# Kernel optimization log

Measured on AMD Instinct MI355X. Metric: run time of the kernel, lower is better.

## Reference

```python
import jax, jax.numpy as jnp
import numpy as np

S_, H_, W_ = 7, 56, 56   # input_resolution
WS = 7                   # window_size
SHIFT = 3                # shift_size
GT = 1                   # gt_num (global tokens per window)
HEADS = 12
EPS = 1e-5


def _rel_pos_index(w):
    # replicates the torch buffer construction (incl. its 3*w-1 / 2*w-1 multipliers)
    coords = np.stack(np.meshgrid(np.arange(w), np.arange(w), np.arange(w), indexing='ij'))
    cf = coords.reshape(3, -1)
    rc = (cf[:, :, None] - cf[:, None, :]).transpose(1, 2, 0).astype(np.int64)
    rc += w - 1
    rc[..., 0] *= 3 * w - 1
    rc[..., 1] *= 2 * w - 1
    return rc.sum(-1)  # (w^3, w^3)


def _attn_mask(S, H, W, w, sh):
    # standard 3D shifted-window mask, built once from static shapes
    img = np.zeros((S, H, W))
    cnt = 0
    sls = (slice(0, -w), slice(-w, -sh), slice(-sh, None))
    for a in sls:
        for b in sls:
            for c in sls:
                img[a, b, c] = cnt
                cnt += 1
    m = img.reshape(S // w, w, H // w, w, W // w, w).transpose(0, 2, 4, 1, 3, 5).reshape(-1, w ** 3)
    d = m[:, None, :] - m[:, :, None]
    return np.where(d != 0, -100.0, 0.0).astype(np.float32)  # (nW, w^3, w^3)


def _ln(x, g, b):
    mu = jnp.mean(x, -1, keepdims=True)
    var = jnp.mean((x - mu) ** 2, -1, keepdims=True)
    return (x - mu) * jax.lax.rsqrt(var + EPS) * g + b


def setup_inputs() -> dict:
    key = jax.random.key(0)
    ks = jax.random.split(key, 7)
    C = 384
    hid = 4 * C
    L = S_ * H_ * W_
    nW = (S_ // WS) * (H_ // WS) * (W_ // WS)
    p = lambda k, shape: jax.random.normal(k, shape, jnp.float32) * 0.02
    return dict(
        x=jax.random.normal(ks[0], (1, L, C), jnp.float32),
        gt=jax.random.normal(ks[1], (nW, GT, C), jnp.float32),
        norm1_g=jnp.ones((C,), jnp.float32), norm1_b=jnp.zeros((C,), jnp.float32),
        qkv_w=p(ks[2], (C, 3 * C)), qkv_b=jnp.zeros((3 * C,), jnp.float32),
        bias_table=p(ks[3], ((2 * WS - 1) ** 3, HEADS)),
        proj_w=p(ks[4], (C, C)), proj_b=jnp.zeros((C,), jnp.float32),
        norm2_g=jnp.ones((C,), jnp.float32), norm2_b=jnp.zeros((C,), jnp.float32),
        fc1_w=p(ks[5], (C, hid)), fc1_b=jnp.zeros((hid,), jnp.float32),
        fc2_w=p(ks[6], (hid, C)), fc2_b=jnp.zeros((C,), jnp.float32),
    )


def _forward(x, gt, norm1_g, norm1_b, qkv_w, qkv_b, bias_table, proj_w, proj_b,
             norm2_g, norm2_b, fc1_w, fc1_b, fc2_w, fc2_b):
    B, L, C = x.shape
    h = HEADS
    d = C // h
    scale = d ** -0.5
    N_ = WS ** 3
    N = N_ + GT
    rpi = _rel_pos_index(WS)
    mask = jnp.asarray(_attn_mask(S_, H_, W_, WS, SHIFT))
    nW = mask.shape[0]

    shortcut = x
    xs = _ln(x, norm1_g, norm1_b).reshape(B, S_, H_, W_, C)
    xs = jnp.roll(xs, (-SHIFT, -SHIFT, -SHIFT), axis=(1, 2, 3))  # cyclic shift
    # window partition -> (B*nW, N_, C)
    xw = xs.reshape(B, S_ // WS, WS, H_ // WS, WS, W_ // WS, WS, C)
    xw = xw.transpose(0, 1, 3, 5, 2, 4, 6, 7).reshape(-1, N_, C)

    # --- WindowAttention with global tokens ---
    xc = jnp.concatenate([gt, xw], axis=1)  # (B*nW, N, C)
    qkv = (xc @ qkv_w + qkv_b).reshape(-1, N, 3, h, d).transpose(2, 0, 3, 1, 4)
    q, k, v = qkv[0] * scale, qkv[1], qkv[2]  # (B*nW, h, N, d)
    attn = jnp.einsum('bhnd,bhmd->bhnm', q, k)
    bias = bias_table[rpi.reshape(-1)].reshape(N_, N_, h).transpose(2, 0, 1)  # (h, N_, N_)
    bias = jnp.pad(bias, ((0, 0), (GT, 0), (GT, 0)))      # zeros on gt rows/cols == original submatrix add
    mpad = jnp.pad(mask, ((0, 0), (GT, 0), (GT, 0)))
    attn = attn + bias[None]
    attn = attn.reshape(B, nW, h, N, N) + mpad[None, :, None]
    attn = jax.nn.softmax(attn.reshape(-1, h, N, N), axis=-1)
    out = jnp.einsum('bhnm,bhmd->bhnd', attn, v).transpose(0, 2, 1, 3).reshape(-1, N, C)
    out = out @ proj_w + proj_b
    gt_out = out[:, :GT]
    xw = out[:, GT:]

    # window reverse + reverse shift
    xs = xw.reshape(B, S_ // WS, H_ // WS, W_ // WS, WS, WS, WS, C)
    xs = xs.transpose(0, 1, 4, 2, 5, 3, 6, 7).reshape(B, S_, H_, W_, C)
    xs = jnp.roll(xs, (SHIFT, SHIFT, SHIFT), axis=(1, 2, 3)).reshape(B, L, C)

    x = shortcut + xs  # drop_path = 0
    y = _ln(x, norm2_g, norm2_b)
    y = jax.nn.gelu(y @ fc1_w + fc1_b, approximate=False) @ fc2_w + fc2_b
    return x + y, gt_out


def reference(x, gt, norm1_g, norm1_b, qkv_w, qkv_b, bias_table, proj_w, proj_b,
              norm2_g, norm2_b, fc1_w, fc1_b, fc2_w, fc2_b):
    return _forward(x, gt, norm1_g, norm1_b, qkv_w, qkv_b, bias_table, proj_w, proj_b,
                    norm2_g, norm2_b, fc1_w, fc1_b, fc2_w, fc2_b)
```

## Files before the change

### kernel.cpp

```cpp
#include <hip/hip_runtime.h>
#include <math.h>

typedef __attribute__((ext_vector_type(8))) short short8;
typedef __attribute__((ext_vector_type(4))) float f32x4;

__device__ __forceinline__ float b2f(short s) {
    unsigned u = ((unsigned)(unsigned short)s) << 16;
    return __builtin_bit_cast(float, u);
}
__device__ __forceinline__ short f2b(float f) {
    unsigned u = __builtin_bit_cast(unsigned, f);
    u += 0x7FFFu + ((u >> 16) & 1u);
    return (short)(u >> 16);
}
__device__ __forceinline__ void gload16(const void* g, void* l) {
    __builtin_amdgcn_global_load_lds(
        (const __attribute__((address_space(1))) unsigned int*)g,
        (__attribute__((address_space(3))) unsigned int*)l, 16, 0, 0);
}

__global__ void transpose_w(const float* __restrict__ src, short* __restrict__ dst,
                            int K, int N) {
    int idx = blockIdx.x * 256 + threadIdx.x;
    if (idx < N * K) {
        int n = idx / K, k = idx - n * K;
        dst[idx] = f2b(src[(size_t)k * N + n]);
    }
}

__global__ void bias_pre(const float* __restrict__ btab, float* __restrict__ btf) {
    int idx = blockIdx.x * 256 + threadIdx.x;
    if (idx >= 12 * 22 * 22 * 64) return;
    int lane = idx & 63, rem = idx >> 6;
    int nb = rem % 22; rem /= 22;
    int rt = rem % 22; int head = rem / 22;
    int j = nb * 16 + (lane & 15);
    int ibase = rt * 16 + (lane >> 4) * 4;
    f32x4 out;
    #pragma unroll
    for (int r = 0; r < 4; r++) {
        int i = ibase + r;
        float v;
        if (j >= 344) v = -1e30f;
        else if (i >= 344 || i == 0 || j == 0) v = 0.f;
        else {
            int ti = i - 1, tj = j - 1;
            int ai = ti / 49, bi = (ti % 49) / 7, ci = ti % 7;
            int aj = tj / 49, bj = (tj % 49) / 7, cj = tj % 7;
            int id3 = (ai - aj + 6) * 20 + (bi - bj + 6) * 13 + (ci - cj + 6);
            v = btab[id3 * 12 + head];
        }
        out[r] = v;
    }
    *(f32x4*)&btf[(size_t)idx * 4] = out;
}

__global__ void gid_pre(unsigned char* __restrict__ gid) {
    int idx = blockIdx.x * 256 + threadIdx.x;
    if (idx >= 64 * 352) return;
    int w = idx / 352, n = idx % 352;
    unsigned char g = 0;
    if (n >= 1 && n < 344) {
        int t = n - 1;
        int a = t / 49, bb = (t % 49) / 7, cc = t % 7;
        int hw = w >> 3, ww = w & 7;
        int h = hw * 7 + bb, wd = ww * 7 + cc;
        int gs = (a < 4) ? 1 : 2;
        int gh = (h < 49) ? 0 : ((h < 53) ? 1 : 2);
        int gw = (wd < 49) ? 0 : ((wd < 53) ? 1 : 2);
        g = (unsigned char)(gs * 9 + gh * 3 + gw);
    }
    gid[idx] = g;
}

__global__ __launch_bounds__(256) void ln1_window(
    const float* __restrict__ x, const float* __restrict__ gt,
    const float* __restrict__ g, const float* __restrict__ b,
    short* __restrict__ xc)
{
    int wid = threadIdx.x >> 6, lane = threadIdx.x & 63;
    int r = blockIdx.x * 4 + wid;
    int w = r / 344, n = r - w * 344;
    if (n == 0) {
        #pragma unroll
        for (int i = 0; i < 6; i++) {
            int c = lane + i * 64;
            xc[(size_t)r * 384 + c] = f2b(gt[(size_t)w * 384 + c]);
        }
        return;
    }
    int t = n - 1;
    int a = t / 49, rm = t - a * 49, bb = rm / 7, cc = rm - bb * 7;
    int hw = w >> 3, ww = w & 7;
    int s = (a < 4) ? a + 3 : a - 4;
    int h = hw * 7 + bb + 3; if (h >= 56) h -= 56;
    int wd = ww * 7 + cc + 3; if (wd >= 56) wd -= 56;
    const float* row = x + (size_t)((s * 56 + h) * 56 + wd) * 384;
    float v[6]; float sum = 0.f;
    #pragma unroll
    for (int i = 0; i < 6; i++) { v[i] = row[lane + i * 64]; sum += v[i]; }
    #pragma unroll
    for (int off = 32; off >= 1; off >>= 1) sum += __shfl_xor(sum, off);
    float mu = sum * (1.0f / 384.0f);
    float vs = 0.f;
    #pragma unroll
    for (int i = 0; i < 6; i++) { float d = v[i] - mu; vs += d * d; }
    #pragma unroll
    for (int off = 32; off >= 1; off >>= 1) vs += __shfl_xor(vs, off);
    float rstd = rsqrtf(vs * (1.0f / 384.0f) + 1e-5f);
    #pragma unroll
    for (int i = 0; i < 6; i++) {
        int c = lane + i * 64;
        float o = (v[i] - mu) * rstd * g[c] + b[c];
        xc[(size_t)r * 384 + c] = f2b(o);
    }
}

__global__ __launch_bounds__(256) void ln2_kernel(
    const float* __restrict__ xn, const float* __restrict__ g,
    const float* __restrict__ b, short* __restrict__ out)
{
    int wid = threadIdx.x >> 6, lane = threadIdx.x & 63;
    int r = blockIdx.x * 4 + wid;
    const float* row = xn + (size_t)r * 384;
    float v[6]; float sum = 0.f;
    #pragma unroll
    for (int i = 0; i < 6; i++) { v[i] = row[lane + i * 64]; sum += v[i]; }
    #pragma unroll
    for (int off = 32; off >= 1; off >>= 1) sum += __shfl_xor(sum, off);
    float mu = sum * (1.0f / 384.0f);
    float vs = 0.f;
    #pragma unroll
    for (int i = 0; i < 6; i++) { float d = v[i] - mu; vs += d * d; }
    #pragma unroll
    for (int off = 32; off >= 1; off >>= 1) vs += __shfl_xor(vs, off);
    float rstd = rsqrtf(vs * (1.0f / 384.0f) + 1e-5f);
    #pragma unroll
    for (int i = 0; i < 6; i++) {
        int c = lane + i * 64;
        float o = (v[i] - mu) * rstd * g[c] + b[c];
        out[(size_t)r * 384 + c] = f2b(o);
    }
}

template<int EPI, bool QS>
__global__ __launch_bounds__(256, 4) void gemm128(
    const short* __restrict__ A, const short* __restrict__ BT,
    const float* __restrict__ bias, void* __restrict__ Out,
    const void* __restrict__ P0, void* __restrict__ P1,
    int M, int N, int K)
{
    __shared__ short As[128 * 64];
    __shared__ short Bs[128 * 64];
    const int m0 = blockIdx.y * 128, n0 = blockIdx.x * 128;
    const int tid = threadIdx.x;
    const int wid = tid >> 6, lane = tid & 63;
    const int wm = wid >> 1, wn = wid & 1;
    const int l15 = lane & 15, quad = lane >> 4;

    f32x4 acc[4][4];
    #pragma unroll
    for (int i = 0; i < 4; i++)
        #pragma unroll
        for (int j = 0; j < 4; j++) acc[i][j] = (f32x4){0.f, 0.f, 0.f, 0.f};

    const int trow = tid >> 3;
    const int cs = tid & 7;
    const int gc = cs ^ (trow & 7);
    const short* Ag[4]; const short* Bg[4];
    #pragma unroll
    for (int j = 0; j < 4; j++) {
        int ar = m0 + j * 32 + trow; if (ar >= M) ar = M - 1;
        Ag[j] = A + (size_t)ar * K + gc * 8;
        Bg[j] = BT + (size_t)(n0 + j * 32 + trow) * K + gc * 8;
    }
    short* AsW[4]; short* BsW[4];
    #pragma unroll
    for (int j = 0; j < 4; j++) {
        AsW[j] = &As[(j * 32 + wid * 8) * 64];
        BsW[j] = &Bs[(j * 32 + wid * 8) * 64];
    }
    int arow[4], brow[4];
    #pragma unroll
    for (int mt = 0; mt < 4; mt++) arow[mt] = wm * 64 + mt * 16 + l15;
    #pragma unroll
    for (int nt = 0; nt < 4; nt++) brow[nt] = wn * 64 + nt * 16 + l15;

    for (int ks = 0; ks < K; ks += 64) {
        #pragma unroll
        for (int j = 0; j < 4; j++) gload16(Ag[j] + ks, AsW[j]);
        #pragma unroll
        for (int j = 0; j < 4; j++) gload16(Bg[j] + ks, BsW[j]);
        __syncthreads();
        #pragma unroll
        for (int ko = 0; ko < 2; ko++) {
            short8 af[4], bf[4];
            #pragma unroll
            for (int mt = 0; mt < 4; mt++)
                af[mt] = *(const short8*)&As[arow[mt] * 64
                         + (((ko * 4 + quad) ^ (l15 & 7)) * 8)];
            #pragma unroll
            for (int nt = 0; nt < 4; nt++)
                bf[nt] = *(const short8*)&Bs[brow[nt] * 64
                         + (((ko * 4 + quad) ^ (l15 & 7)) * 8)];
            #pragma unroll
            for (int mt = 0; mt < 4; mt++)
                #pragma unroll
                for (int nt = 0; nt < 4; nt++)
                    acc[mt][nt] = __builtin_amdgcn_mfma_f32_16x16x32_bf16(
                        af[mt], bf[nt], acc[mt][nt], 0, 0, 0);
        }
        __syncthreads();
    }

    #pragma unroll
    for (int mt = 0; mt < 4; mt++) {
        #pragma unroll
        for (int nt = 0; nt < 4; nt++) {
            #pragma unroll
            for (int r = 0; r < 4; r++) {
                int row = m0 + wm * 64 + mt * 16 + quad * 4 + r;
                int col = n0 + wn * 64 + nt * 16 + l15;
                if (row >= M) continue;
                float v = acc[mt][nt][r] + bias[col];
                if (EPI == 0) {
                    if (QS && col < 384) v *= 0.17677669529663687f;
                    ((short*)Out)[(size_t)row * N + col] = f2b(v);
                } else if (EPI == 1) {
                    v = 0.5f * v * (1.0f + erff(v * 0.7071067811865476f));
                    ((short*)Out)[(size_t)row * N + col] = f2b(v);
                } else if (EPI == 2) {
                    int w = row / 344, n = row - w * 344;
                    if (n == 0) {
                        ((float*)P1)[(size_t)w * 384 + col] = v;
                    } else {
                        int t = n - 1;
                        int a = t / 49, rm = t - a * 49;
                        int bb = rm / 7, cc = rm - bb * 7;
                        int hw = w >> 3, ww = w & 7;
                        int s = (a < 4) ? a + 3 : a - 4;
                        int h = hw * 7 + bb + 3; if (h >= 56) h -= 56;
                        int wd = ww * 7 + cc + 3; if (wd >= 56) wd -= 56;
                        size_t td = (size_t)((s * 56 + h) * 56 + wd) * 384 + col;
                        ((float*)Out)[td] = v + ((const float*)P0)[td];
                    }
                } else {
                    v += ((const float*)P0)[(size_t)row * N + col];
                    ((float*)Out)[(size_t)row * N + col] = v;
                }
            }
        }
    }
}

__global__ __launch_bounds__(256) void attn_kernel(
    const short* __restrict__ qkv, const float* __restrict__ btf,
    const unsigned char* __restrict__ gid, short* __restrict__ attn_out)
{
    __shared__ short KT[352 * 40];
    __shared__ short VT[32 * 360];
    __shared__ short Pbuf[4 * 16 * 40];
    __shared__ unsigned char Gs[352];
    const int blk = blockIdx.x;
    const int half = blk & 1, wh = blk >> 1;
    const int w = wh / 12, head = wh - w * 12;
    const int tid = threadIdx.x;
    const int wid = tid >> 6, lane = tid & 63;
    const int l15 = lane & 15, quad = lane >> 4;
    const size_t base = (size_t)w * 344 * 1152 + head * 32;

    for (int c = tid; c < 352 * 4; c += 256) {
        int row = c >> 2, off = (c & 3) * 8;
        short8 v8 = (short8){0,0,0,0,0,0,0,0};
        if (row < 344) v8 = *(const short8*)&qkv[base + 384 + (size_t)row * 1152 + off];
        *(short8*)&KT[row * 40 + off] = v8;
    }
    for (int e = tid; e < 344 * 32; e += 256) {
        int key = e >> 5, dd = e & 31;
        VT[dd * 360 + key] = qkv[base + 768 + (size_t)key * 1152 + dd];
    }
    for (int e = tid; e < 16 * 32; e += 256) {
        int key = 344 + (e >> 5), dd = e & 31;
        VT[dd * 360 + key] = 0;
    }
    for (int e = tid; e < 352; e += 256) Gs[e] = gid[w * 352 + e];
    __syncthreads();

    const float* bh = btf + (size_t)head * (22 * 22 * 256);
    short* Pw = &Pbuf[wid * 640];

    for (int rtl = wid; rtl < 11; rtl += 4) {
        int rt = half * 11 + rtl;
        int mbase = rt * 16;
        int qr = mbase + l15; if (qr > 343) qr = 343;
        short8 af = *(const short8*)&qkv[base + (size_t)qr * 1152 + quad * 8];

        int rg[4]; bool ip[4];
        #pragma unroll
        for (int r = 0; r < 4; r++) {
            int i = mbase + quad * 4 + r;
            rg[r] = Gs[i];
            ip[r] = (i > 0);
        }

        f32x4 o0 = {0.f, 0.f, 0.f, 0.f}, o1 = {0.f, 0.f, 0.f, 0.f};
        float l[4] = {0.f, 0.f, 0.f, 0.f};

        #pragma unroll
        for (int kk = 0; kk < 11; kk++) {
            int nb0 = kk * 2, nb1 = kk * 2 + 1;
            f32x4 b0 = *(const f32x4*)&bh[((size_t)(rt * 22 + nb0) * 64 + lane) * 4];
            f32x4 b1 = *(const f32x4*)&bh[((size_t)(rt * 22 + nb1) * 64 + lane) * 4];
            short8 k0 = *(const short8*)&KT[(nb0 * 16 + l15) * 40 + quad * 8];
            short8 k1 = *(const short8*)&KT[(nb1 * 16 + l15) * 40 + quad * 8];
            f32x4 s0 = __builtin_amdgcn_mfma_f32_16x16x32_bf16(af, k0, b0, 0, 0, 0);
            f32x4 s1 = __builtin_amdgcn_mfma_f32_16x16x32_bf16(af, k1, b1, 0, 0, 0);

            int j0 = nb0 * 16 + l15;
            int cg0 = Gs[j0], cg1 = Gs[j0 + 16];
            bool jp0 = (j0 > 0);
            #pragma unroll
            for (int r = 0; r < 4; r++) {
                float s0r = s0[r], s1r = s1[r];
                if (jp0 && ip[r] && rg[r] != cg0) s0r -= 100.0f;
                if (ip[r] && rg[r] != cg1) s1r -= 100.0f;
                float p0 = __expf(s0r);
                float p1 = __expf(s1r);
                l[r] += p0 + p1;
                Pw[(quad * 4 + r) * 40 + l15] = f2b(p0);
                Pw[(quad * 4 + r) * 40 + 16 + l15] = f2b(p1);
            }
            short8 pa = *(const short8*)&Pw[l15 * 40 + quad * 8];
            short8 v0 = *(const short8*)&VT[l15 * 360 + kk * 32 + quad * 8];
            short8 v1 = *(const short8*)&VT[(16 + l15) * 360 + kk * 32 + quad * 8];
            o0 = __builtin_amdgcn_mfma_f32_16x16x32_bf16(pa, v0, o0, 0, 0, 0);
            o1 = __builtin_amdgcn_mfma_f32_16x16x32_bf16(pa, v1, o1, 0, 0, 0);
        }

        #pragma unroll
        for (int r = 0; r < 4; r++) {
            l[r] += __shfl_xor(l[r], 1);
            l[r] += __shfl_xor(l[r], 2);
            l[r] += __shfl_xor(l[r], 4);
            l[r] += __shfl_xor(l[r], 8);
        }
        #pragma unroll
        for (int r = 0; r < 4; r++) {
            int row = mbase + quad * 4 + r;
            if (row < 344) {
                float inv = 1.0f / l[r];
                size_t ob = ((size_t)w * 344 + row) * 384 + head * 32;
                attn_out[ob + l15] = f2b(o0[r] * inv);
                attn_out[ob + 16 + l15] = f2b(o1[r] * inv);
            }
        }
    }
}

extern "C" void kernel_launch(void* const* d_in, const int* in_sizes, int n_in,
                              void* d_out, int out_size, void* d_ws, size_t ws_size,
                              hipStream_t stream)
{
    const float* x      = (const float*)d_in[0];
    const float* gt     = (const float*)d_in[1];
    const float* n1g    = (const float*)d_in[2];
    const float* n1b    = (const float*)d_in[3];
    const float* qkv_w  = (const float*)d_in[4];
    const float* qkv_b  = (const float*)d_in[5];
    const float* btab   = (const float*)d_in[6];
    const float* proj_w = (const float*)d_in[7];
    const float* proj_b = (const float*)d_in[8];
    const float* n2g    = (const float*)d_in[9];
    const float* n2b    = (const float*)d_in[10];
    const float* fc1_w  = (const float*)d_in[11];
    const float* fc1_b  = (const float*)d_in[12];
    const float* fc2_w  = (const float*)d_in[13];
    const float* fc2_b  = (const float*)d_in[14];

    char* ws = (char*)d_ws;
    short* wt_qkv  = (short*)(ws + 0);
    short* wt_proj = (short*)(ws + 884736);
    short* wt_fc1  = (short*)(ws + 1179648);
    short* wt_fc2  = (short*)(ws + 2359296);
    short* xc      = (short*)(ws + 3538944);
    short* qkvb    = (short*)(ws + 20447232);
    short* attn_o  = xc;
    short* h1      = (short*)(ws + 3538944);
    float* xnew    = (float*)(ws + 71172096);
    float* btf     = (float*)(ws + 71172096);
    unsigned char* gidb = (unsigned char*)(ws + 77119488);
    short* xnorm   = (short*)(ws + 104890368);

    float* outx  = (float*)d_out;
    float* outgt = outx + (size_t)21952 * 384;

    transpose_w<<<dim3((442368 + 255) / 256), 256, 0, stream>>>(qkv_w, wt_qkv, 384, 1152);
    transpose_w<<<dim3((147456 + 255) / 256), 256, 0, stream>>>(proj_w, wt_proj, 384, 384);
    transpose_w<<<dim3((589824 + 255) / 256), 256, 0, stream>>>(fc1_w, wt_fc1, 384, 1536);
    transpose_w<<<dim3((589824 + 255) / 256), 256, 0, stream>>>(fc2_w, wt_fc2, 1536, 384);

    bias_pre<<<dim3((12 * 22 * 22 * 64 + 255) / 256), 256, 0, stream>>>(btab, btf);
    gid_pre<<<dim3((64 * 352 + 255) / 256), 256, 0, stream>>>(gidb);

    ln1_window<<<dim3(5504), 256, 0, stream>>>(x, gt, n1g, n1b, xc);

    gemm128<0, true><<<dim3(9, 172), 256, 0, stream>>>(xc, wt_qkv, qkv_b, qkvb,
                                                       nullptr, nullptr, 22016, 1152, 384);

    attn_kernel<<<dim3(1536), 256, 0, stream>>>(qkvb, btf, gidb, attn_o);

    gemm128<2, false><<<dim3(3, 172), 256, 0, stream>>>(attn_o, wt_proj, proj_b, xnew,
                                                        x, outgt, 22016, 384, 384);

    ln2_kernel<<<dim3(5488), 256, 0, stream>>>(xnew, n2g, n2b, xnorm);

    gemm128<1, false><<<dim3(12, 172), 256, 0, stream>>>(xnorm, wt_fc1, fc1_b, h1,
                                                         nullptr, nullptr, 21952, 1536, 384);

    gemm128<3, false><<<dim3(3, 172), 256, 0, stream>>>(h1, wt_fc2, fc2_b, outx,
                                                        xnew, nullptr, 21952, 384, 1536);
}
```

Before: 441.6 us.

## Double-buffer LDS tiles in gemm128 to overlap global loads with MFMA

Doubles the shared-memory A/B tiles and prefetches the next K-slice with global_load_lds while the current slice is consumed by MFMAs. Manual vmcnt/lgkmcnt waits and raw barriers replace __syncthreads. Occupancy hint drops from 4 to 2 blocks per CU because LDS usage doubles, trading parallelism for latency hiding.

```diff
diff --git a/kernel.cpp b/kernel.cpp
--- a/kernel.cpp
+++ b/kernel.cpp
@@ -144,14 +144,14 @@
 }
 
 template<int EPI, bool QS>
-__global__ __launch_bounds__(256, 4) void gemm128(
+__global__ __launch_bounds__(256, 2) void gemm128(
     const short* __restrict__ A, const short* __restrict__ BT,
     const float* __restrict__ bias, void* __restrict__ Out,
     const void* __restrict__ P0, void* __restrict__ P1,
     int M, int N, int K)
 {
-    __shared__ short As[128 * 64];
-    __shared__ short Bs[128 * 64];
+    __shared__ short As[2 * 128 * 64];
+    __shared__ short Bs[2 * 128 * 64];
     const int m0 = blockIdx.y * 128, n0 = blockIdx.x * 128;
     const int tid = threadIdx.x;
     const int wid = tid >> 6, lane = tid & 63;
@@ -186,22 +186,41 @@
     #pragma unroll
     for (int nt = 0; nt < 4; nt++) brow[nt] = wn * 64 + nt * 16 + l15;
 
-    for (int ks = 0; ks < K; ks += 64) {
-        #pragma unroll
-        for (int j = 0; j < 4; j++) gload16(Ag[j] + ks, AsW[j]);
-        #pragma unroll
-        for (int j = 0; j < 4; j++) gload16(Bg[j] + ks, BsW[j]);
-        __syncthreads();
+    const int nsteps = K >> 6;
+
+    #pragma unroll
+    for (int j = 0; j < 4; j++) gload16(Ag[j], AsW[j]);
+    #pragma unroll
+    for (int j = 0; j < 4; j++) gload16(Bg[j], BsW[j]);
+
+    int cur = 0;
+    for (int t = 0; t < nsteps; ++t) {
+        if (t + 1 < nsteps) {
+            const int nb = (cur ^ 1) << 13;
+            const int ksn = (t + 1) << 6;
+            #pragma unroll
+            for (int j = 0; j < 4; j++) gload16(Ag[j] + ksn, AsW[j] + nb);
+            #pragma unroll
+            for (int j = 0; j < 4; j++) gload16(Bg[j] + ksn, BsW[j] + nb);
+            asm volatile("s_waitcnt vmcnt(8)" ::: "memory");
+        } else {
+            asm volatile("s_waitcnt vmcnt(0)" ::: "memory");
+        }
+        __builtin_amdgcn_s_barrier();
+        asm volatile("" ::: "memory");
+
+        const short* Ab = &As[cur << 13];
+        const short* Bb = &Bs[cur << 13];
         #pragma unroll
         for (int ko = 0; ko < 2; ko++) {
             short8 af[4], bf[4];
             #pragma unroll
             for (int mt = 0; mt < 4; mt++)
-                af[mt] = *(const short8*)&As[arow[mt] * 64
+                af[mt] = *(const short8*)&Ab[arow[mt] * 64
                          + (((ko * 4 + quad) ^ (l15 & 7)) * 8)];
             #pragma unroll
             for (int nt = 0; nt < 4; nt++)
-                bf[nt] = *(const short8*)&Bs[brow[nt] * 64
+                bf[nt] = *(const short8*)&Bb[brow[nt] * 64
                          + (((ko * 4 + quad) ^ (l15 & 7)) * 8)];
             #pragma unroll
             for (int mt = 0; mt < 4; mt++)
@@ -210,7 +229,9 @@
                     acc[mt][nt] = __builtin_amdgcn_mfma_f32_16x16x32_bf16(
                         af[mt], bf[nt], acc[mt][nt], 0, 0, 0);
         }
-        __syncthreads();
+        asm volatile("s_waitcnt lgkmcnt(0)" ::: "memory");
+        __builtin_amdgcn_s_barrier();
+        cur ^= 1;
     }
 
     #pragma unroll
```

Result: slower. 637.8 us (+44.4%).
